# Kernel optimization log

Hardware: AMD Instinct MI355X
Metric: run time of the kernel (lower is better)

## Reference

```python
import jax, jax.numpy as jnp
import numpy as np

B, T, IMG, P, D, H, L = 4, 32, 84, 14, 768, 12, 3
GP = IMG // P            # 6 patches per side
NP = GP * GP             # 36 patches
N = NP + 1               # +cls token
FF = 4 * D
HD = D // H


def _ln(x, g, b):
    m = jnp.mean(x, -1, keepdims=True)
    v = jnp.var(x, -1, keepdims=True)
    return (x - m) * jax.lax.rsqrt(v + 1e-5) * g + b


def _mha(x, qkv_w, qkv_b, proj_w, proj_b):
    Bn, Nn, C = x.shape
    qkv = (x @ qkv_w + qkv_b).reshape(Bn, Nn, 3, H, HD).transpose(2, 0, 3, 1, 4)
    q, k, v = qkv[0], qkv[1], qkv[2]                      # (B,H,N,hd)
    attn = jax.nn.softmax(jnp.einsum('bhqd,bhkd->bhqk', q, k) * HD ** -0.5, axis=-1)
    o = jnp.einsum('bhqk,bhkd->bhqd', attn, v).transpose(0, 2, 1, 3).reshape(Bn, Nn, C)
    return o @ proj_w + proj_b


def _blocks(x, pre_g, pre_b, n1_g, n1_b, qkv_w, qkv_b, proj_w, proj_b,
            n2_g, n2_b, fc1_w, fc1_b, fc2_w, fc2_b):
    # TemporalViT applies an extra pre-norm, then x = x + Block(x_norm),
    # where Block itself contains two residual sublayers on x_norm.
    for i in range(L):
        xn = _ln(x, pre_g[i], pre_b[i])
        y = xn + _mha(_ln(xn, n1_g[i], n1_b[i]), qkv_w[i], qkv_b[i], proj_w[i], proj_b[i])
        h = jax.nn.gelu(_ln(y, n2_g[i], n2_b[i]) @ fc1_w[i] + fc1_b[i], approximate=False)
        y = y + h @ fc2_w[i] + fc2_b[i]
        x = x + y
    return x


def _forward(x, conv_w, conv_b, cls, pos, tpos,
             s_pre_g, s_pre_b, s_n1_g, s_n1_b, s_qkv_w, s_qkv_b, s_proj_w, s_proj_b,
             s_n2_g, s_n2_b, s_fc1_w, s_fc1_b, s_fc2_w, s_fc2_b,
             t_pre_g, t_pre_b, t_n1_g, t_n1_b, t_qkv_w, t_qkv_b, t_proj_w, t_proj_b,
             t_n2_g, t_n2_b, t_fc1_w, t_fc1_b, t_fc2_w, t_fc2_b):
    xf = x.reshape(B * T, 3, IMG, IMG)
    p = jax.lax.conv_general_dilated(xf, conv_w, (P, P), 'VALID',
                                     dimension_numbers=('NCHW', 'OIHW', 'NCHW'))
    p = p + conv_b[None, :, None, None]                  # (BT, D, 6, 6)
    p = p.reshape(B * T, D, NP).transpose(0, 2, 1)       # (BT, 36, D)
    p = jnp.concatenate([jnp.broadcast_to(cls, (B * T, 1, D)), p], axis=1) + pos
    p = _blocks(p, s_pre_g, s_pre_b, s_n1_g, s_n1_b, s_qkv_w, s_qkv_b, s_proj_w,
                s_proj_b, s_n2_g, s_n2_b, s_fc1_w, s_fc1_b, s_fc2_w, s_fc2_b)
    p = p.reshape(B, T * N, D)
    tp = jnp.broadcast_to(tpos[:, :T, None, :], (1, T, N, D)).reshape(1, T * N, D)
    p = p + tp
    p = _blocks(p, t_pre_g, t_pre_b, t_n1_g, t_n1_b, t_qkv_w, t_qkv_b, t_proj_w,
                t_proj_b, t_n2_g, t_n2_b, t_fc1_w, t_fc1_b, t_fc2_w, t_fc2_b)
    return p.mean(axis=1)                                # (B, D)


def setup_inputs() -> dict:
    key = jax.random.key(0)
    ks = iter(jax.random.split(key, 64))
    r = lambda shape, s=0.02: (jax.random.normal(next(ks), shape, jnp.float32) * s)
    inp = {
        'x': jax.random.normal(next(ks), (B, T, 3, IMG, IMG), jnp.float32),
        'conv_w': r((D, 3, P, P)), 'conv_b': jnp.zeros((D,), jnp.float32),
        'cls': r((1, 1, D)), 'pos': r((1, N, D)), 'tpos': r((1, 100, D)),
    }
    for pfx in ('s', 't'):
        inp[f'{pfx}_pre_g'] = jnp.ones((L, D), jnp.float32)
        inp[f'{pfx}_pre_b'] = jnp.zeros((L, D), jnp.float32)
        inp[f'{pfx}_n1_g'] = jnp.ones((L, D), jnp.float32)
        inp[f'{pfx}_n1_b'] = jnp.zeros((L, D), jnp.float32)
        inp[f'{pfx}_qkv_w'] = r((L, D, 3 * D))
        inp[f'{pfx}_qkv_b'] = jnp.zeros((L, 3 * D), jnp.float32)
        inp[f'{pfx}_proj_w'] = r((L, D, D))
        inp[f'{pfx}_proj_b'] = jnp.zeros((L, D), jnp.float32)
        inp[f'{pfx}_n2_g'] = jnp.ones((L, D), jnp.float32)
        inp[f'{pfx}_n2_b'] = jnp.zeros((L, D), jnp.float32)
        inp[f'{pfx}_fc1_w'] = r((L, D, FF))
        inp[f'{pfx}_fc1_b'] = jnp.zeros((L, FF), jnp.float32)
        inp[f'{pfx}_fc2_w'] = r((L, FF, D))
        inp[f'{pfx}_fc2_b'] = jnp.zeros((L, D), jnp.float32)
    return inp


def reference(x, conv_w, conv_b, cls, pos, tpos,
              s_pre_g, s_pre_b, s_n1_g, s_n1_b, s_qkv_w, s_qkv_b, s_proj_w, s_proj_b,
              s_n2_g, s_n2_b, s_fc1_w, s_fc1_b, s_fc2_w, s_fc2_b,
              t_pre_g, t_pre_b, t_n1_g, t_n1_b, t_qkv_w, t_qkv_b, t_proj_w, t_proj_b,
              t_n2_g, t_n2_b, t_fc1_w, t_fc1_b, t_fc2_w, t_fc2_b):
    return _forward(x, conv_w, conv_b, cls, pos, tpos,
                    s_pre_g, s_pre_b, s_n1_g, s_n1_b, s_qkv_w, s_qkv_b, s_proj_w,
                    s_proj_b, s_n2_g, s_n2_b, s_fc1_w, s_fc1_b, s_fc2_w, s_fc2_b,
                    t_pre_g, t_pre_b, t_n1_g, t_n1_b, t_qkv_w, t_qkv_b, t_proj_w,
                    t_proj_b, t_n2_g, t_n2_b, t_fc1_w, t_fc1_b, t_fc2_w, t_fc2_b)
```

## Files before the change

kernel.cpp:

```cpp
#include <hip/hip_runtime.h>
#include <math.h>

#define NTOK 4736
#define DM   768
#define NHEAD 12
#define KC   640

typedef __attribute__((ext_vector_type(8))) short bf16x8;
typedef __attribute__((ext_vector_type(4))) float f32x4;

__device__ inline short f2bf(float f) {
  union { float f; unsigned u; } v; v.f = f;
  unsigned r = v.u + 0x7FFF + ((v.u >> 16) & 1);
  return (short)(r >> 16);
}

__device__ inline void gload16(const void* g, void* l) {
  __builtin_amdgcn_global_load_lds(
      (const __attribute__((address_space(1))) void*)g,
      (__attribute__((address_space(3))) void*)l, 16, 0, 0);
}

__global__ __launch_bounds__(256) void im2col_k(const float* __restrict__ x,
                                                short* __restrict__ col) {
  int i = blockIdx.x * 256 + threadIdx.x;
  int r = i / KC, k = i % KC;
  short v = 0;
  if (k < 588) {
    int bt = r / 36, p = r % 36;
    int gy = p / 6, gx = p % 6;
    int c = k / 196, rem = k % 196;
    int ky = rem / 14, kx = rem % 14;
    v = f2bf(x[(((size_t)bt * 3 + c) * 84 + gy * 14 + ky) * 84 + gx * 14 + kx]);
  }
  col[i] = v;
}

__global__ __launch_bounds__(256) void convw_k(const float* __restrict__ w,
                                               short* __restrict__ out) {
  int i = blockIdx.x * 256 + threadIdx.x;
  int n = i / KC, k = i % KC;
  out[i] = (k < 588) ? f2bf(w[(size_t)n * 588 + k]) : (short)0;
}

__global__ __launch_bounds__(256) void wt_k(const float* __restrict__ in,
                                            short* __restrict__ out,
                                            int K, int N) {
  __shared__ float tile[32][33];
  const int l = blockIdx.z;
  in  += (size_t)l * K * N;
  out += (size_t)l * N * K;
  const int n0 = blockIdx.x * 32, k0 = blockIdx.y * 32;
  const int tx = threadIdx.x & 31, ty = threadIdx.x >> 5;
#pragma unroll
  for (int r = 0; r < 4; r++)
    tile[ty + 8 * r][tx] = in[(size_t)(k0 + ty + 8 * r) * N + n0 + tx];
  __syncthreads();
#pragma unroll
  for (int r = 0; r < 4; r++)
    out[(size_t)(n0 + ty + 8 * r) * K + k0 + tx] = f2bf(tile[tx][ty + 8 * r]);
}

__global__ __launch_bounds__(256) void assemble_k(const float* __restrict__ conv_out,
                                                  const float* __restrict__ cls,
                                                  const float* __restrict__ pos,
                                                  float* __restrict__ X) {
  int i = blockIdx.x * 256 + threadIdx.x;
  int t = i / DM, d = i % DM;
  int bt = t / 37, n = t % 37;
  float v = (n == 0) ? cls[d] : conv_out[((size_t)bt * 36 + (n - 1)) * DM + d];
  X[i] = v + pos[n * DM + d];
}

__global__ __launch_bounds__(256) void tpos_k(float* __restrict__ X,
                                              const float* __restrict__ tpos) {
  int i = blockIdx.x * 256 + threadIdx.x;
  int row = i / DM, d = i % DM;
  int tt = (row % 1184) / 37;
  X[i] += tpos[tt * DM + d];
}

template <bool OBF>
__global__ __launch_bounds__(256) void ln_k(const float* __restrict__ in,
                                            const float* __restrict__ g,
                                            const float* __restrict__ b,
                                            void* __restrict__ outp) {
  int r = blockIdx.x;
  int tid = threadIdx.x;
  const float* xr = in + (size_t)r * DM;
  float v0 = xr[tid], v1 = xr[tid + 256], v2 = xr[tid + 512];
  float s  = v0 + v1 + v2;
  float sq = v0 * v0 + v1 * v1 + v2 * v2;
#pragma unroll
  for (int off = 32; off; off >>= 1) {
    s  += __shfl_down(s, off);
    sq += __shfl_down(sq, off);
  }
  __shared__ float ss[4], sg[4];
  if ((tid & 63) == 0) { ss[tid >> 6] = s; sg[tid >> 6] = sq; }
  __syncthreads();
  float S = ss[0] + ss[1] + ss[2] + ss[3];
  float Q = sg[0] + sg[1] + sg[2] + sg[3];
  float mean = S * (1.f / 768.f);
  float var  = Q * (1.f / 768.f) - mean * mean;
  float rs = rsqrtf(var + 1e-5f);
  float o0 = (v0 - mean) * rs * g[tid]       + b[tid];
  float o1 = (v1 - mean) * rs * g[tid + 256] + b[tid + 256];
  float o2 = (v2 - mean) * rs * g[tid + 512] + b[tid + 512];
  if (OBF) {
    short* o = (short*)outp + (size_t)r * DM;
    o[tid] = f2bf(o0); o[tid + 256] = f2bf(o1); o[tid + 512] = f2bf(o2);
  } else {
    float* o = (float*)outp + (size_t)r * DM;
    o[tid] = o0; o[tid + 256] = o1; o[tid + 512] = o2;
  }
}

__global__ __launch_bounds__(256) void ln2_k(const float* __restrict__ in,
                                             const float* __restrict__ g1,
                                             const float* __restrict__ b1,
                                             const float* __restrict__ g2,
                                             const float* __restrict__ b2,
                                             float* __restrict__ xn,
                                             short* __restrict__ w) {
  int r = blockIdx.x;
  int tid = threadIdx.x;
  const float* xr = in + (size_t)r * DM;
  float v0 = xr[tid], v1 = xr[tid + 256], v2 = xr[tid + 512];
  float s  = v0 + v1 + v2;
  float sq = v0 * v0 + v1 * v1 + v2 * v2;
#pragma unroll
  for (int off = 32; off; off >>= 1) {
    s  += __shfl_down(s, off);
    sq += __shfl_down(sq, off);
  }
  __shared__ float ss[4], sg[4], ss2[4], sg2[4];
  if ((tid & 63) == 0) { ss[tid >> 6] = s; sg[tid >> 6] = sq; }
  __syncthreads();
  float S = ss[0] + ss[1] + ss[2] + ss[3];
  float Q = sg[0] + sg[1] + sg[2] + sg[3];
  float mean = S * (1.f / 768.f);
  float var  = Q * (1.f / 768.f) - mean * mean;
  float rs = rsqrtf(var + 1e-5f);
  float x0 = (v0 - mean) * rs * g1[tid]       + b1[tid];
  float x1 = (v1 - mean) * rs * g1[tid + 256] + b1[tid + 256];
  float x2 = (v2 - mean) * rs * g1[tid + 512] + b1[tid + 512];
  float* xo = xn + (size_t)r * DM;
  xo[tid] = x0; xo[tid + 256] = x1; xo[tid + 512] = x2;
  float s2  = x0 + x1 + x2;
  float sq2 = x0 * x0 + x1 * x1 + x2 * x2;
#pragma unroll
  for (int off = 32; off; off >>= 1) {
    s2  += __shfl_down(s2, off);
    sq2 += __shfl_down(sq2, off);
  }
  if ((tid & 63) == 0) { ss2[tid >> 6] = s2; sg2[tid >> 6] = sq2; }
  __syncthreads();
  float S2 = ss2[0] + ss2[1] + ss2[2] + ss2[3];
  float Q2 = sg2[0] + sg2[1] + sg2[2] + sg2[3];
  float mean2 = S2 * (1.f / 768.f);
  float var2  = Q2 * (1.f / 768.f) - mean2 * mean2;
  float rs2 = rsqrtf(var2 + 1e-5f);
  short* wo = w + (size_t)r * DM;
  wo[tid]       = f2bf((x0 - mean2) * rs2 * g2[tid]       + b2[tid]);
  wo[tid + 256] = f2bf((x1 - mean2) * rs2 * g2[tid + 256] + b2[tid + 256]);
  wo[tid + 512] = f2bf((x2 - mean2) * rs2 * g2[tid + 512] + b2[tid + 512]);
}

template <int BM, int BN, int WM, int WN, bool BMFAST, bool GELU, bool OBF,
          bool HASR1, bool HASR2>
__global__ __launch_bounds__(256, 2) void tgemm_k(const short* __restrict__ A,
                                                  const short* __restrict__ Bw,
                                                  const float* __restrict__ bias,
                                                  const float* __restrict__ r1,
                                                  const float* __restrict__ r2,
                                                  void* __restrict__ Cout,
                                                  int M, int N, int K) {
  constexpr int TM = BM / WM, TN = BN / WN;
  constexpr int MF = TM / 16, NF = TN / 16;
  constexpr int RPC = 32;
  constexpr int ACH = BM / RPC, BCH = BN / RPC;
  constexpr int LOADS = ACH + BCH;

  __shared__ short As[2][BM][64];
  __shared__ short Bs[2][BN][64];

  const int nwg  = gridDim.x * gridDim.y;
  const int orig = blockIdx.x + gridDim.x * blockIdx.y;
  const int qq = nwg >> 3, rr = nwg & 7;
  const int xcd = orig & 7, sub = orig >> 3;
  const int wgid = ((xcd < rr) ? xcd * (qq + 1) : rr * (qq + 1) + (xcd - rr) * qq) + sub;
  int bm, bn;
  if (BMFAST) { bm = (wgid % gridDim.x) * BM; bn = (wgid / gridDim.x) * BN; }
  else        { bm = (wgid / gridDim.y) * BM; bn = (wgid % gridDim.y) * BN; }

  const int tid = threadIdx.x, wid = tid >> 6, lane = tid & 63;
  const int lr = lane & 15, lg = lane >> 4;
  const int wm = wid / WN, wn = wid % WN;

  const int srow = tid >> 3;
  const int sslot = (tid & 7) ^ (srow & 7);
  const short* Asrc = A  + (size_t)(bm + srow) * K + sslot * 8;
  const short* Bsrc = Bw + (size_t)(bn + srow) * K + sslot * 8;

  f32x4 acc[MF][NF];
#pragma unroll
  for (int m = 0; m < MF; m++)
#pragma unroll
    for (int n = 0; n < NF; n++) acc[m][n] = (f32x4){0.f, 0.f, 0.f, 0.f};

#define STAGE(slot, kk)                                                        \
  do {                                                                         \
    _Pragma("unroll")                                                          \
    for (int j = 0; j < ACH; j++)                                              \
      gload16(Asrc + (size_t)(j * RPC) * K + (kk),                             \
              (char*)&As[slot][0][0] + j * RPC * 128 + wid * 1024);            \
    _Pragma("unroll")                                                          \
    for (int j = 0; j < BCH; j++)                                              \
      gload16(Bsrc + (size_t)(j * RPC) * K + (kk),                             \
              (char*)&Bs[slot][0][0] + j * RPC * 128 + wid * 1024);            \
  } while (0)

  const int NT = K >> 6;
  const int swz = (lr & 7) << 4;

  STAGE(0, 0);
  for (int t = 0; t < NT; t++) {
    const int c = t & 1;
    if (t + 1 < NT) STAGE(c ^ 1, (t + 1) << 6);
    if (t + 1 < NT) {
      if constexpr (LOADS == 8)      asm volatile("s_waitcnt vmcnt(8)" ::: "memory");
      else if constexpr (LOADS == 6) asm volatile("s_waitcnt vmcnt(6)" ::: "memory");
      else                           asm volatile("s_waitcnt vmcnt(0)" ::: "memory");
    } else {
      asm volatile("s_waitcnt vmcnt(0)" ::: "memory");
    }
    __builtin_amdgcn_s_barrier();

    bf16x8 bq[NF][2], aq[MF][2];
#pragma unroll
    for (int nf = 0; nf < NF; nf++) {
      const int row = wn * TN + nf * 16 + lr;
#pragma unroll
      for (int ks = 0; ks < 2; ks++)
        bq[nf][ks] = *reinterpret_cast<const bf16x8*>(
            (const char*)&Bs[c][0][0] + row * 128 + ((ks * 64 + lg * 16) ^ swz));
    }
#pragma unroll
    for (int mf = 0; mf < MF; mf++) {
      const int row = wm * TM + mf * 16 + lr;
#pragma unroll
      for (int ks = 0; ks < 2; ks++)
        aq[mf][ks] = *reinterpret_cast<const bf16x8*>(
            (const char*)&As[c][0][0] + row * 128 + ((ks * 64 + lg * 16) ^ swz));
    }
    __builtin_amdgcn_s_setprio(1);
#pragma unroll
    for (int mf = 0; mf < MF; mf++)
#pragma unroll
      for (int nf = 0; nf < NF; nf++) {
        acc[mf][nf] = __builtin_amdgcn_mfma_f32_16x16x32_bf16(
            aq[mf][0], bq[nf][0], acc[mf][nf], 0, 0, 0);
        acc[mf][nf] = __builtin_amdgcn_mfma_f32_16x16x32_bf16(
            aq[mf][1], bq[nf][1], acc[mf][nf], 0, 0, 0);
      }
    __builtin_amdgcn_s_setprio(0);
    __builtin_amdgcn_s_barrier();
  }
#undef STAGE

#pragma unroll
  for (int m = 0; m < MF; m++) {
#pragma unroll
    for (int r = 0; r < 4; r++) {
      int row = bm + wm * TM + m * 16 + lg * 4 + r;
      if (row < M) {
#pragma unroll
        for (int n = 0; n < NF; n++) {
          int col = bn + wn * TN + n * 16 + lr;
          size_t idx = (size_t)row * N + col;
          float v = acc[m][n][r];
          if (bias) v += bias[col];
          if (GELU) v = 0.5f * v * (1.f + erff(v * 0.70710678118654752f));
          if (HASR1) v += r1[idx];
          if (HASR2) v += r2[idx];
          if (OBF) ((short*)Cout)[idx] = f2bf(v);
          else     ((float*)Cout)[idx] = v;
        }
      }
    }
  }
}

__global__ __launch_bounds__(256) void attn_k(const short* __restrict__ qkv,
                                              short* __restrict__ out,
                                              int Bn, int Nn) {
  const int gx = gridDim.x, gy = gridDim.y;
  const int nwg = gx * gy;
  const int orig = blockIdx.x + gx * blockIdx.y;
  const int qq = nwg >> 3, rr = nwg & 7;
  const int xcd = orig & 7, sub = orig >> 3;
  const int wgid = ((xcd < rr) ? xcd * (qq + 1) : rr * (qq + 1) + (xcd - rr) * qq) + sub;
  const int bh = wgid / gy;
  const int qb = wgid % gy;
  const int b = bh / NHEAD, h = bh % NHEAD;
  const int q0 = qb * 64;

  const int tid = threadIdx.x;
  const int wid = tid >> 6, lane = tid & 63;
  const int lr = lane & 15, lg = lane >> 4;

  __shared__ short Ks[64][64];
  __shared__ short Vt[64][64];
  __shared__ short Ps[4][16][64];

  const int qrow_in = q0 + wid * 16 + lr;
  const int qcl = (qrow_in < Nn) ? qrow_in : (Nn - 1);
  const short* qp = qkv + ((size_t)(b * Nn + qcl)) * 2304 + h * 64 + lg * 8;
  bf16x8 qa0 = *reinterpret_cast<const bf16x8*>(qp);
  bf16x8 qa1 = *reinterpret_cast<const bf16x8*>(qp + 32);

  f32x4 oo[4];
#pragma unroll
  for (int dg = 0; dg < 4; dg++) oo[dg] = (f32x4){0.f, 0.f, 0.f, 0.f};
  float mm[4] = {-1e30f, -1e30f, -1e30f, -1e30f};
  float ll[4] = {0.f, 0.f, 0.f, 0.f};

  const int skey = tid >> 2;
  const int sdq  = (tid & 3) * 16;
  const int vkey = tid & 63;
  const int vd0  = wid * 16;

  const int swr = (lr & 7) << 3;

  for (int k0 = 0; k0 < Nn; k0 += 64) {
    {
      int kg = k0 + skey; if (kg >= Nn) kg = Nn - 1;
      const short* kp = qkv + ((size_t)(b * Nn + kg)) * 2304 + 768 + h * 64 + sdq;
      bf16x8 ka = *reinterpret_cast<const bf16x8*>(kp);
      bf16x8 kb = *reinterpret_cast<const bf16x8*>(kp + 8);
      const int ksw = (skey & 7) << 3;
      *reinterpret_cast<bf16x8*>(&Ks[skey][sdq ^ ksw])       = ka;
      *reinterpret_cast<bf16x8*>(&Ks[skey][(sdq + 8) ^ ksw]) = kb;
      int vg = k0 + vkey; if (vg >= Nn) vg = Nn - 1;
      const short* vp = qkv + ((size_t)(b * Nn + vg)) * 2304 + 1536 + h * 64 + vd0;
      bf16x8 va = *reinterpret_cast<const bf16x8*>(vp);
      bf16x8 vb = *reinterpret_cast<const bf16x8*>(vp + 8);
#pragma unroll
      for (int i = 0; i < 8; i++) {
        Vt[vd0 + i][vkey ^ (i << 3)]     = va[i];
        Vt[vd0 + 8 + i][vkey ^ (i << 3)] = vb[i];
      }
    }
    __syncthreads();

    f32x4 c[4];
#pragma unroll
    for (int kf = 0; kf < 4; kf++) {
      c[kf] = (f32x4){0.f, 0.f, 0.f, 0.f};
      const short* krow = &Ks[kf * 16 + lr][0];
      bf16x8 kb0 = *reinterpret_cast<const bf16x8*>(krow + ((lg * 8) ^ swr));
      c[kf] = __builtin_amdgcn_mfma_f32_16x16x32_bf16(qa0, kb0, c[kf], 0, 0, 0);
      bf16x8 kb1 = *reinterpret_cast<const bf16x8*>(krow + ((32 + lg * 8) ^ swr));
      c[kf] = __builtin_amdgcn_mfma_f32_16x16x32_bf16(qa1, kb1, c[kf], 0, 0, 0);
    }
#pragma unroll
    for (int kf = 0; kf < 4; kf++) {
#pragma unroll
      for (int r = 0; r < 4; r++) c[kf][r] *= 0.125f;
      if (k0 + kf * 16 + lr >= Nn)
        c[kf][0] = c[kf][1] = c[kf][2] = c[kf][3] = -1e30f;
    }

    float tr[4];
#pragma unroll
    for (int r = 0; r < 4; r++) {
      float t = fmaxf(fmaxf(c[0][r], c[1][r]), fmaxf(c[2][r], c[3][r]));
      t = fmaxf(t, __shfl_xor(t, 1, 16));
      t = fmaxf(t, __shfl_xor(t, 2, 16));
      t = fmaxf(t, __shfl_xor(t, 4, 16));
      t = fmaxf(t, __shfl_xor(t, 8, 16));
      tr[r] = t;
    }
    const bool skipall = __all((tr[0] - mm[0] <= 8.f) & (tr[1] - mm[1] <= 8.f) &
                               (tr[2] - mm[2] <= 8.f) & (tr[3] - mm[3] <= 8.f));
#pragma unroll
    for (int r = 0; r < 4; r++) {
      if (!skipall) {
        float mn = fmaxf(mm[r], tr[r]);
        float sc = __expf(mm[r] - mn);
        ll[r] *= sc;
        oo[0][r] *= sc; oo[1][r] *= sc; oo[2][r] *= sc; oo[3][r] *= sc;
        mm[r] = mn;
      }
      float p0 = __expf(c[0][r] - mm[r]);
      float p1 = __expf(c[1][r] - mm[r]);
      float p2 = __expf(c[2][r] - mm[r]);
      float p3 = __expf(c[3][r] - mm[r]);
      float ps = (p0 + p1) + (p2 + p3);
      ps += __shfl_xor(ps, 1, 16);
      ps += __shfl_xor(ps, 2, 16);
      ps += __shfl_xor(ps, 4, 16);
      ps += __shfl_xor(ps, 8, 16);
      ll[r] += ps;
      const int prow = lg * 4 + r;
      const int psw  = (prow & 7) << 3;
      short* pr = &Ps[wid][prow][0];
      pr[lr ^ psw]        = f2bf(p0);
      pr[(16 + lr) ^ psw] = f2bf(p1);
      pr[(32 + lr) ^ psw] = f2bf(p2);
      pr[(48 + lr) ^ psw] = f2bf(p3);
    }

#pragma unroll
    for (int ks = 0; ks < 2; ks++) {
      bf16x8 pa = *reinterpret_cast<const bf16x8*>(&Ps[wid][lr][(ks * 32 + lg * 8) ^ swr]);
#pragma unroll
      for (int dg = 0; dg < 4; dg++) {
        bf16x8 vb = *reinterpret_cast<const bf16x8*>(
            &Vt[dg * 16 + lr][(ks * 32 + lg * 8) ^ swr]);
        oo[dg] = __builtin_amdgcn_mfma_f32_16x16x32_bf16(pa, vb, oo[dg], 0, 0, 0);
      }
    }
    __syncthreads();
  }

#pragma unroll
  for (int r = 0; r < 4; r++) {
    int qr = q0 + wid * 16 + lg * 4 + r;
    if (qr < Nn) {
      float inv = 1.f / ll[r];
      short* op = out + ((size_t)(b * Nn + qr)) * DM + h * 64 + lr;
      op[0]  = f2bf(oo[0][r] * inv);
      op[16] = f2bf(oo[1][r] * inv);
      op[32] = f2bf(oo[2][r] * inv);
      op[48] = f2bf(oo[3][r] * inv);
    }
  }
}

__global__ __launch_bounds__(256) void mean1_k(const float* __restrict__ X,
                                               float* __restrict__ P) {
  int b = blockIdx.x, seg = blockIdx.z;
  int d = blockIdx.y * 256 + threadIdx.x;
  int r0 = seg * 148;
  float s = 0.f;
  for (int r = r0; r < r0 + 148; r++) s += X[((size_t)b * 1184 + r) * DM + d];
  P[((size_t)(b * 8 + seg)) * DM + d] = s;
}
__global__ __launch_bounds__(256) void mean2_k(const float* __restrict__ P,
                                               float* __restrict__ out) {
  int b = blockIdx.x;
  int d = blockIdx.y * 256 + threadIdx.x;
  float s = 0.f;
#pragma unroll
  for (int seg = 0; seg < 8; seg++) s += P[((size_t)(b * 8 + seg)) * DM + d];
  out[b * DM + d] = s * (1.f / 1184.f);
}

extern "C" void kernel_launch(void* const* d_in, const int* in_sizes, int n_in,
                              void* d_out, int out_size, void* d_ws, size_t ws_size,
                              hipStream_t stream) {
  (void)in_sizes; (void)n_in; (void)out_size; (void)ws_size;
  const float* x      = (const float*)d_in[0];
  const float* conv_w = (const float*)d_in[1];
  const float* conv_b = (const float*)d_in[2];
  const float* cls    = (const float*)d_in[3];
  const float* pos    = (const float*)d_in[4];
  const float* tpos   = (const float*)d_in[5];
  const float* W[2][14];
  for (int p = 0; p < 2; p++)
    for (int i = 0; i < 14; i++)
      W[p][i] = (const float*)d_in[6 + p * 14 + i];

  char* ws = (char*)d_ws;
  const size_t TOKF = (size_t)NTOK * DM * 4;
  float* X    = (float*)(ws);
  float* XN   = (float*)(ws + TOKF);
  float* Y    = (float*)(ws + 2 * TOKF);
  short* TA2  = (short*)(ws + 3 * TOKF);
  short* BIG  = (short*)(ws + 3 * TOKF + (size_t)NTOK * DM * 2);
  short* WB   = (short*)(ws + 3 * TOKF + (size_t)NTOK * DM * 2
                            + (size_t)NTOK * 3072 * 2);
  const size_t QE = (size_t)3 * 2304 * 768;
  const size_t PE = (size_t)3 * 768 * 768;
  const size_t F1E = (size_t)3 * 3072 * 768;
  const size_t F2E = (size_t)3 * 768 * 3072;
  const size_t PFX = QE + PE + F1E + F2E;
  short* WQ[2], *WP[2], *WF1[2], *WF2[2];
  for (int p = 0; p < 2; p++) {
    WQ[p]  = WB + p * PFX;
    WP[p]  = WQ[p] + QE;
    WF1[p] = WP[p] + PE;
    WF2[p] = WF1[p] + F1E;
  }
  short* CW = WB + 2 * PFX;
  float* PB = (float*)(CW + (size_t)768 * KC);

  for (int p = 0; p < 2; p++) {
    wt_k<<<dim3(72, 24, 3), 256, 0, stream>>>(W[p][4],  WQ[p],  768, 2304);
    wt_k<<<dim3(24, 24, 3), 256, 0, stream>>>(W[p][6],  WP[p],  768, 768);
    wt_k<<<dim3(96, 24, 3), 256, 0, stream>>>(W[p][10], WF1[p], 768, 3072);
    wt_k<<<dim3(24, 96, 3), 256, 0, stream>>>(W[p][12], WF2[p], 3072, 768);
  }
  convw_k<<<1920, 256, 0, stream>>>(conv_w, CW);

  im2col_k<<<11520, 256, 0, stream>>>(x, BIG);
  tgemm_k<64, 128, 1, 4, false, false, false, false, false>
      <<<dim3(72, 6), 256, 0, stream>>>(
      BIG, CW, conv_b, nullptr, nullptr, Y, 4608, 768, KC);
  assemble_k<<<14208, 256, 0, stream>>>(Y, cls, pos, X);

  for (int phase = 0; phase < 2; phase++) {
    const int Bn = (phase == 0) ? 128 : 4;
    const int Nn = (phase == 0) ? 37 : 1184;
    if (phase == 1) tpos_k<<<14208, 256, 0, stream>>>(X, tpos);
    for (int i = 0; i < 3; i++) {
      const float* pre_g = W[phase][0] + i * DM;
      const float* pre_b = W[phase][1] + i * DM;
      const float* n1_g  = W[phase][2] + i * DM;
      const float* n1_b  = W[phase][3] + i * DM;
      const float* qkv_b = W[phase][5] + i * 2304;
      const float* prj_b = W[phase][7] + i * DM;
      const float* n2_g  = W[phase][8] + i * DM;
      const float* n2_b  = W[phase][9] + i * DM;
      const float* fc1_b = W[phase][11] + i * 3072;
      const float* fc2_b = W[phase][13] + i * DM;
      const short* qkv_w = WQ[phase]  + (size_t)i * 2304 * 768;
      const short* prj_w = WP[phase]  + (size_t)i * 768 * 768;
      const short* fc1_w = WF1[phase] + (size_t)i * 3072 * 768;
      const short* fc2_w = WF2[phase] + (size_t)i * 768 * 3072;

      ln2_k<<<NTOK, 256, 0, stream>>>(X, pre_g, pre_b, n1_g, n1_b, XN, TA2);
      tgemm_k<128, 128, 2, 2, false, false, true, false, false>
          <<<dim3(37, 18), 256, 0, stream>>>(
          TA2, qkv_w, qkv_b, nullptr, nullptr, BIG, NTOK, 2304, DM);
      attn_k<<<dim3(Bn * NHEAD, (Nn + 63) / 64), 256, 0, stream>>>(BIG, TA2, Bn, Nn);
      tgemm_k<64, 128, 1, 4, false, false, false, true, false>
          <<<dim3(74, 6), 256, 0, stream>>>(
          TA2, prj_w, prj_b, XN, nullptr, Y, NTOK, DM, DM);
      ln_k<true><<<NTOK, 256, 0, stream>>>(Y, n2_g, n2_b, TA2);
      tgemm_k<128, 128, 2, 2, true, true, true, false, false>
          <<<dim3(37, 24), 256, 0, stream>>>(
          TA2, fc1_w, fc1_b, nullptr, nullptr, BIG, NTOK, 3072, DM);
      tgemm_k<64, 128, 1, 4, true, false, false, true, true>
          <<<dim3(74, 6), 256, 0, stream>>>(
          BIG, fc2_w, fc2_b, Y, X, X, NTOK, DM, 3072);
    }
  }
  mean1_k<<<dim3(4, 3, 8), 256, 0, stream>>>(X, PB);
  mean2_k<<<dim3(4, 3), 256, 0, stream>>>(PB, (float*)d_out);
}
```

Before: 1.696 ms.

## Halve GEMM K-tile to 32, use 2x2 warps, smaller N tiles, higher occupancy

The GEMM kernel now stages 32-wide K slices instead of 64, with a new 4-slot XOR swizzle and a single MFMA per fragment pair per step. That halves the LDS footprint, and launch bounds request 4 workgroups per CU instead of 2. The narrow-N GEMMs (conv, proj, fc2) switch from 64x128 tiles with a 1x4 warp layout to 64x64 tiles with 2x2 warps, doubling the grid. The aim is more occupancy and better wave fill, at the cost of more barriers per K and less reuse per tile.

```diff
diff --git a/kernel.cpp b/kernel.cpp
--- a/kernel.cpp
+++ b/kernel.cpp
@@ -167,39 +167,35 @@
   wo[tid + 512] = f2bf((x2 - mean2) * rs2 * g2[tid + 512] + b2[tid + 512]);
 }
 
-template <int BM, int BN, int WM, int WN, bool BMFAST, bool GELU, bool OBF,
-          bool HASR1, bool HASR2>
-__global__ __launch_bounds__(256, 2) void tgemm_k(const short* __restrict__ A,
+template <int BM, int BN, bool GELU, bool OBF, bool HASR1, bool HASR2>
+__global__ __launch_bounds__(256, 4) void tgemm_k(const short* __restrict__ A,
                                                   const short* __restrict__ Bw,
                                                   const float* __restrict__ bias,
                                                   const float* __restrict__ r1,
                                                   const float* __restrict__ r2,
                                                   void* __restrict__ Cout,
                                                   int M, int N, int K) {
-  constexpr int TM = BM / WM, TN = BN / WN;
+  constexpr int TM = BM / 2, TN = BN / 2;
   constexpr int MF = TM / 16, NF = TN / 16;
-  constexpr int RPC = 32;
-  constexpr int ACH = BM / RPC, BCH = BN / RPC;
+  constexpr int ACH = BM / 64, BCH = BN / 64;
   constexpr int LOADS = ACH + BCH;
 
-  __shared__ short As[2][BM][64];
-  __shared__ short Bs[2][BN][64];
+  __shared__ short As[2][BM][32];
+  __shared__ short Bs[2][BN][32];
 
   const int nwg  = gridDim.x * gridDim.y;
   const int orig = blockIdx.x + gridDim.x * blockIdx.y;
-  const int qq = nwg >> 3, rr = nwg & 7;
+  const int qq = nwg >> 3, rrm = nwg & 7;
   const int xcd = orig & 7, sub = orig >> 3;
-  const int wgid = ((xcd < rr) ? xcd * (qq + 1) : rr * (qq + 1) + (xcd - rr) * qq) + sub;
-  int bm, bn;
-  if (BMFAST) { bm = (wgid % gridDim.x) * BM; bn = (wgid / gridDim.x) * BN; }
-  else        { bm = (wgid / gridDim.y) * BM; bn = (wgid % gridDim.y) * BN; }
+  const int wgid = ((xcd < rrm) ? xcd * (qq + 1) : rrm * (qq + 1) + (xcd - rrm) * qq) + sub;
+  const int bm = (wgid / gridDim.y) * BM, bn = (wgid % gridDim.y) * BN;
 
   const int tid = threadIdx.x, wid = tid >> 6, lane = tid & 63;
   const int lr = lane & 15, lg = lane >> 4;
-  const int wm = wid / WN, wn = wid % WN;
-
-  const int srow = tid >> 3;
-  const int sslot = (tid & 7) ^ (srow & 7);
+  const int wm = wid >> 1, wn = wid & 1;
+
+  const int srow = tid >> 2;
+  const int sslot = (tid & 3) ^ ((srow >> 1) & 3);
   const short* Asrc = A  + (size_t)(bm + srow) * K + sslot * 8;
   const short* Bsrc = Bw + (size_t)(bn + srow) * K + sslot * 8;
 
@@ -213,57 +209,49 @@
   do {                                                                         \
     _Pragma("unroll")                                                          \
     for (int j = 0; j < ACH; j++)                                              \
-      gload16(Asrc + (size_t)(j * RPC) * K + (kk),                             \
-              (char*)&As[slot][0][0] + j * RPC * 128 + wid * 1024);            \
+      gload16(Asrc + (size_t)(j * 64) * K + (kk),                              \
+              (char*)&As[slot][0][0] + j * 4096 + wid * 1024);                 \
     _Pragma("unroll")                                                          \
     for (int j = 0; j < BCH; j++)                                              \
-      gload16(Bsrc + (size_t)(j * RPC) * K + (kk),                             \
-              (char*)&Bs[slot][0][0] + j * RPC * 128 + wid * 1024);            \
+      gload16(Bsrc + (size_t)(j * 64) * K + (kk),                              \
+              (char*)&Bs[slot][0][0] + j * 4096 + wid * 1024);                 \
   } while (0)
 
-  const int NT = K >> 6;
-  const int swz = (lr & 7) << 4;
+  const int NT = K >> 5;
+  const int rkey = (lr >> 1) & 3;
 
   STAGE(0, 0);
   for (int t = 0; t < NT; t++) {
     const int c = t & 1;
-    if (t + 1 < NT) STAGE(c ^ 1, (t + 1) << 6);
     if (t + 1 < NT) {
-      if constexpr (LOADS == 8)      asm volatile("s_waitcnt vmcnt(8)" ::: "memory");
-      else if constexpr (LOADS == 6) asm volatile("s_waitcnt vmcnt(6)" ::: "memory");
-      else                           asm volatile("s_waitcnt vmcnt(0)" ::: "memory");
+      STAGE(c ^ 1, (t + 1) << 5);
+      if constexpr (LOADS == 4) asm volatile("s_waitcnt vmcnt(4)" ::: "memory");
+      else                      asm volatile("s_waitcnt vmcnt(2)" ::: "memory");
     } else {
       asm volatile("s_waitcnt vmcnt(0)" ::: "memory");
     }
     __builtin_amdgcn_s_barrier();
 
-    bf16x8 bq[NF][2], aq[MF][2];
+    bf16x8 aq[MF], bq[NF];
 #pragma unroll
     for (int nf = 0; nf < NF; nf++) {
       const int row = wn * TN + nf * 16 + lr;
-#pragma unroll
-      for (int ks = 0; ks < 2; ks++)
-        bq[nf][ks] = *reinterpret_cast<const bf16x8*>(
-            (const char*)&Bs[c][0][0] + row * 128 + ((ks * 64 + lg * 16) ^ swz));
+      bq[nf] = *reinterpret_cast<const bf16x8*>(
+          (const char*)&Bs[c][0][0] + row * 64 + ((lg ^ rkey) << 4));
     }
 #pragma unroll
     for (int mf = 0; mf < MF; mf++) {
       const int row = wm * TM + mf * 16 + lr;
-#pragma unroll
-      for (int ks = 0; ks < 2; ks++)
-        aq[mf][ks] = *reinterpret_cast<const bf16x8*>(
-            (const char*)&As[c][0][0] + row * 128 + ((ks * 64 + lg * 16) ^ swz));
+      aq[mf] = *reinterpret_cast<const bf16x8*>(
+          (const char*)&As[c][0][0] + row * 64 + ((lg ^ rkey) << 4));
     }
     __builtin_amdgcn_s_setprio(1);
 #pragma unroll
     for (int mf = 0; mf < MF; mf++)
 #pragma unroll
-      for (int nf = 0; nf < NF; nf++) {
+      for (int nf = 0; nf < NF; nf++)
         acc[mf][nf] = __builtin_amdgcn_mfma_f32_16x16x32_bf16(
-            aq[mf][0], bq[nf][0], acc[mf][nf], 0, 0, 0);
-        acc[mf][nf] = __builtin_amdgcn_mfma_f32_16x16x32_bf16(
-            aq[mf][1], bq[nf][1], acc[mf][nf], 0, 0, 0);
-      }
+            aq[mf], bq[nf], acc[mf][nf], 0, 0, 0);
     __builtin_amdgcn_s_setprio(0);
     __builtin_amdgcn_s_barrier();
   }
@@ -298,9 +286,9 @@
   const int gx = gridDim.x, gy = gridDim.y;
   const int nwg = gx * gy;
   const int orig = blockIdx.x + gx * blockIdx.y;
-  const int qq = nwg >> 3, rr = nwg & 7;
+  const int qq = nwg >> 3, rrm = nwg & 7;
   const int xcd = orig & 7, sub = orig >> 3;
-  const int wgid = ((xcd < rr) ? xcd * (qq + 1) : rr * (qq + 1) + (xcd - rr) * qq) + sub;
+  const int wgid = ((xcd < rrm) ? xcd * (qq + 1) : rrm * (qq + 1) + (xcd - rrm) * qq) + sub;
   const int bh = wgid / gy;
   const int qb = wgid % gy;
   const int b = bh / NHEAD, h = bh % NHEAD;
@@ -506,8 +494,7 @@
   convw_k<<<1920, 256, 0, stream>>>(conv_w, CW);
 
   im2col_k<<<11520, 256, 0, stream>>>(x, BIG);
-  tgemm_k<64, 128, 1, 4, false, false, false, false, false>
-      <<<dim3(72, 6), 256, 0, stream>>>(
+  tgemm_k<64, 64, false, false, false, false><<<dim3(72, 12), 256, 0, stream>>>(
       BIG, CW, conv_b, nullptr, nullptr, Y, 4608, 768, KC);
   assemble_k<<<14208, 256, 0, stream>>>(Y, cls, pos, X);
 
@@ -532,19 +519,15 @@
       const short* fc2_w = WF2[phase] + (size_t)i * 768 * 3072;
 
       ln2_k<<<NTOK, 256, 0, stream>>>(X, pre_g, pre_b, n1_g, n1_b, XN, TA2);
-      tgemm_k<128, 128, 2, 2, false, false, true, false, false>
-          <<<dim3(37, 18), 256, 0, stream>>>(
+      tgemm_k<128, 128, false, true, false, false><<<dim3(37, 18), 256, 0, stream>>>(
           TA2, qkv_w, qkv_b, nullptr, nullptr, BIG, NTOK, 2304, DM);
       attn_k<<<dim3(Bn * NHEAD, (Nn + 63) / 64), 256, 0, stream>>>(BIG, TA2, Bn, Nn);
-      tgemm_k<64, 128, 1, 4, false, false, false, true, false>
-          <<<dim3(74, 6), 256, 0, stream>>>(
+      tgemm_k<64, 64, false, false, true, false><<<dim3(74, 12), 256, 0, stream>>>(
           TA2, prj_w, prj_b, XN, nullptr, Y, NTOK, DM, DM);
       ln_k<true><<<NTOK, 256, 0, stream>>>(Y, n2_g, n2_b, TA2);
-      tgemm_k<128, 128, 2, 2, true, true, true, false, false>
-          <<<dim3(37, 24), 256, 0, stream>>>(
+      tgemm_k<128, 128, true, true, false, false><<<dim3(37, 24), 256, 0, stream>>>(
           TA2, fc1_w, fc1_b, nullptr, nullptr, BIG, NTOK, 3072, DM);
-      tgemm_k<64, 128, 1, 4, true, false, false, true, true>
-          <<<dim3(74, 6), 256, 0, stream>>>(
+      tgemm_k<64, 64, false, false, true, true><<<dim3(74, 12), 256, 0, stream>>>(
           BIG, fc2_w, fc2_b, Y, X, X, NTOK, DM, 3072);
     }
   }
```

Result: faster. 1.504 ms (-11.3%).
